# Optimization experiments

Hardware: AMD Instinct MI355X
Metric: run time of the kernel (lower is better)

The kernel has to match this reference:

```python
import jax, jax.numpy as jnp
import numpy as np

NUM_HEADS = 16

def setup_inputs() -> dict:
    key = jax.random.key(0)
    k1, k2, k3 = jax.random.split(key, 3)
    B, S, D = 4, 4096, 2048
    q = jax.random.normal(k1, (B, S, D), dtype=jnp.float32)
    k = jax.random.normal(k2, (B, S, D), dtype=jnp.float32)
    v = jax.random.normal(k3, (B, S, D), dtype=jnp.float32)
    # buffer: decay per head, shape (1, num_heads, 1), default 0.9 per head
    decay = jnp.full((1, NUM_HEADS, 1), 0.9, dtype=jnp.float32)
    return {"q": q, "k": k, "v": v, "decay": decay}

def reference(q, k, v, decay):
    B, S, D = q.shape
    H = NUM_HEADS
    hd = D // H
    qh = q.reshape(B, S, H, hd)
    kh = k.reshape(B, S, H, hd)
    vh = v.reshape(B, S, H, hd)
    kv = kh * vh                       # [B,S,H,hd] per-step state increment
    kv_t = jnp.moveaxis(kv, 1, 0)      # [S,B,H,hd] scan over time
    d = decay                          # [1,H,1], broadcasts over (B,H,hd)

    def step(r, inc):
        r = d * r + inc                # r: [B,H,hd]
        return r, r

    r0 = jnp.zeros((B, H, hd), dtype=q.dtype)
    _, rs = jax.lax.scan(step, r0, kv_t)   # rs: [S,B,H,hd]
    out = qh * jnp.moveaxis(rs, 0, 1)      # [B,S,H,hd]
    return out.reshape(B, S, D)
```

## Files before the change

### kernel.cpp

```cpp
#include <hip/hip_runtime.h>


namespace {

constexpr int kBlk  = 256;
constexpr int kB    = 4;
constexpr int kS    = 4096;
constexpr int kD    = 2048;
constexpr int kRow  = kD / 4;
constexpr int kNG   = kB * kRow;
constexpr int kC    = 64;
constexpr int kL    = kS / kC;

__global__ __launch_bounds__(kBlk) void chunk_state_kernel(
    const float4* __restrict__ k, const float4* __restrict__ v,
    const float* __restrict__ decay, float4* __restrict__ A) {
  const int tid = blockIdx.x * kBlk + threadIdx.x;
  const int g   = tid & (kNG - 1);
  const int c   = tid >> 11;
  const int b   = g >> 9;
  const int j4  = g & (kRow - 1);
  const int h   = j4 >> 5;
  const float d = decay[h];

  int base = (b * kS + c * kL) * kRow + j4;
  float4 r = make_float4(0.f, 0.f, 0.f, 0.f);
#pragma unroll 4
  for (int i = 0; i < kL; ++i) {
    float4 kk = k[base + i * kRow];
    float4 vv = v[base + i * kRow];
    r.x = fmaf(d, r.x, kk.x * vv.x);
    r.y = fmaf(d, r.y, kk.y * vv.y);
    r.z = fmaf(d, r.z, kk.z * vv.z);
    r.w = fmaf(d, r.w, kk.w * vv.w);
  }
  A[c * kNG + g] = r;
}

__global__ __launch_bounds__(kBlk) void retention_out_kernel(
    const float4* __restrict__ q, const float4* __restrict__ k,
    const float4* __restrict__ v, const float* __restrict__ decay,
    const float4* __restrict__ A, float4* __restrict__ out) {
  const int tid = blockIdx.x * kBlk + threadIdx.x;
  const int g   = tid & (kNG - 1);
  const int c   = tid >> 11;
  const int b   = g >> 9;
  const int j4  = g & (kRow - 1);
  const int h   = j4 >> 5;
  const float d = decay[h];

  float dL = d;
#pragma unroll
  for (int t = 0; t < 6; ++t) dL *= dL;

  float4 r = make_float4(0.f, 0.f, 0.f, 0.f);
  for (int cc = 0; cc < c; ++cc) {
    float4 a = A[cc * kNG + g];
    r.x = fmaf(dL, r.x, a.x);
    r.y = fmaf(dL, r.y, a.y);
    r.z = fmaf(dL, r.z, a.z);
    r.w = fmaf(dL, r.w, a.w);
  }

  int base = (b * kS + c * kL) * kRow + j4;
#pragma unroll 4
  for (int i = 0; i < kL; ++i) {
    float4 qq = q[base + i * kRow];
    float4 kk = k[base + i * kRow];
    float4 vv = v[base + i * kRow];
    r.x = fmaf(d, r.x, kk.x * vv.x);
    r.y = fmaf(d, r.y, kk.y * vv.y);
    r.z = fmaf(d, r.z, kk.z * vv.z);
    r.w = fmaf(d, r.w, kk.w * vv.w);
    float4 o;
    o.x = qq.x * r.x;
    o.y = qq.y * r.y;
    o.z = qq.z * r.z;
    o.w = qq.w * r.w;
    out[base + i * kRow] = o;
  }
}

}

extern "C" void kernel_launch(void* const* d_in, const int* in_sizes, int n_in,
                              void* d_out, int out_size, void* d_ws, size_t ws_size,
                              hipStream_t stream) {
  const float4* q     = (const float4*)d_in[0];
  const float4* k     = (const float4*)d_in[1];
  const float4* v     = (const float4*)d_in[2];
  const float*  decay = (const float*)d_in[3];
  float4* out = (float4*)d_out;
  float4* A   = (float4*)d_ws;

  const int nthreads = kNG * kC;
  const int nblocks  = nthreads / kBlk;

  chunk_state_kernel<<<nblocks, kBlk, 0, stream>>>(k, v, decay, A);
  retention_out_kernel<<<nblocks, kBlk, 0, stream>>>(q, k, v, decay, A, out);
}
```

Measured before the change: 442.7 us.

## Shrink scan chunks to 16 steps and truncate decayed cross-chunk prefix

Chunk length drops from 64 to 16 timesteps, so both kernels launch four times as many threads and hide memory latency better. The prefix over earlier chunk states is cut off once the accumulated decay falls below about 1e-10. That bound is computed at run time from the decay value, so each thread reads only a few chunk states instead of up to all of them. The hot loops are manually unrolled with loads grouped ahead of use, and occupancy hints are added to the launch bounds. In exchange, the workspace for chunk states grows fourfold, with a fallback to 64-step chunks if the workspace is too small. Dropping terms below the cutoff gives a tiny approximation error.

```diff
diff --git a/kernel.cpp b/kernel.cpp
--- a/kernel.cpp
+++ b/kernel.cpp
@@ -3,16 +3,15 @@
 
 namespace {
 
-constexpr int kBlk  = 256;
-constexpr int kB    = 4;
-constexpr int kS    = 4096;
-constexpr int kD    = 2048;
-constexpr int kRow  = kD / 4;
-constexpr int kNG   = kB * kRow;
-constexpr int kC    = 64;
-constexpr int kL    = kS / kC;
+constexpr int kBlk = 256;
+constexpr int kB   = 4;
+constexpr int kS   = 4096;
+constexpr int kD   = 2048;
+constexpr int kRow = kD / 4;
+constexpr int kNG  = kB * kRow;
 
-__global__ __launch_bounds__(kBlk) void chunk_state_kernel(
+template <int KL>
+__global__ __launch_bounds__(kBlk, 8) void chunk_state_kernel(
     const float4* __restrict__ k, const float4* __restrict__ v,
     const float* __restrict__ decay, float4* __restrict__ A) {
   const int tid = blockIdx.x * kBlk + threadIdx.x;
@@ -20,24 +19,39 @@
   const int c   = tid >> 11;
   const int b   = g >> 9;
   const int j4  = g & (kRow - 1);
-  const int h   = j4 >> 5;
-  const float d = decay[h];
+  const float d = decay[j4 >> 5];
 
-  int base = (b * kS + c * kL) * kRow + j4;
+  const float4* kp = k + (b * kS + c * KL) * kRow + j4;
+  const float4* vp = v + (b * kS + c * KL) * kRow + j4;
   float4 r = make_float4(0.f, 0.f, 0.f, 0.f);
 #pragma unroll 4
-  for (int i = 0; i < kL; ++i) {
-    float4 kk = k[base + i * kRow];
-    float4 vv = v[base + i * kRow];
-    r.x = fmaf(d, r.x, kk.x * vv.x);
-    r.y = fmaf(d, r.y, kk.y * vv.y);
-    r.z = fmaf(d, r.z, kk.z * vv.z);
-    r.w = fmaf(d, r.w, kk.w * vv.w);
+  for (int ii = 0; ii < KL / 4; ++ii) {
+    float4 k0 = kp[0 * kRow], k1 = kp[1 * kRow], k2 = kp[2 * kRow], k3 = kp[3 * kRow];
+    float4 v0 = vp[0 * kRow], v1 = vp[1 * kRow], v2 = vp[2 * kRow], v3 = vp[3 * kRow];
+    kp += 4 * kRow;
+    vp += 4 * kRow;
+    r.x = fmaf(d, r.x, k0.x * v0.x);
+    r.y = fmaf(d, r.y, k0.y * v0.y);
+    r.z = fmaf(d, r.z, k0.z * v0.z);
+    r.w = fmaf(d, r.w, k0.w * v0.w);
+    r.x = fmaf(d, r.x, k1.x * v1.x);
+    r.y = fmaf(d, r.y, k1.y * v1.y);
+    r.z = fmaf(d, r.z, k1.z * v1.z);
+    r.w = fmaf(d, r.w, k1.w * v1.w);
+    r.x = fmaf(d, r.x, k2.x * v2.x);
+    r.y = fmaf(d, r.y, k2.y * v2.y);
+    r.z = fmaf(d, r.z, k2.z * v2.z);
+    r.w = fmaf(d, r.w, k2.w * v2.w);
+    r.x = fmaf(d, r.x, k3.x * v3.x);
+    r.y = fmaf(d, r.y, k3.y * v3.y);
+    r.z = fmaf(d, r.z, k3.z * v3.z);
+    r.w = fmaf(d, r.w, k3.w * v3.w);
   }
   A[c * kNG + g] = r;
 }
 
-__global__ __launch_bounds__(kBlk) void retention_out_kernel(
+template <int KL>
+__global__ __launch_bounds__(kBlk, 4) void retention_out_kernel(
     const float4* __restrict__ q, const float4* __restrict__ k,
     const float4* __restrict__ v, const float* __restrict__ decay,
     const float4* __restrict__ A, float4* __restrict__ out) {
@@ -46,38 +60,71 @@
   const int c   = tid >> 11;
   const int b   = g >> 9;
   const int j4  = g & (kRow - 1);
-  const int h   = j4 >> 5;
-  const float d = decay[h];
+  const float d = decay[j4 >> 5];
 
   float dL = d;
+  constexpr int kLog = (KL == 16) ? 4 : 6;
 #pragma unroll
-  for (int t = 0; t < 6; ++t) dL *= dL;
+  for (int t = 0; t < kLog; ++t) dL *= dL;
+
+  int n = c;
+  if (c > 0 && dL < 0.999999f) {
+    float l = __logf(fmaxf(dL, 1e-37f));
+    int need = (int)ceilf(-23.0259f / l);
+    n = need < 1 ? 1 : (need < c ? need : c);
+  }
 
   float4 r = make_float4(0.f, 0.f, 0.f, 0.f);
-  for (int cc = 0; cc < c; ++cc) {
-    float4 a = A[cc * kNG + g];
+  const float4* ap = A + (c - n) * kNG + g;
+#pragma unroll 2
+  for (int i = 0; i < n; ++i) {
+    float4 a = ap[0];
+    ap += kNG;
     r.x = fmaf(dL, r.x, a.x);
     r.y = fmaf(dL, r.y, a.y);
     r.z = fmaf(dL, r.z, a.z);
     r.w = fmaf(dL, r.w, a.w);
   }
 
-  int base = (b * kS + c * kL) * kRow + j4;
+  const int base = (b * kS + c * KL) * kRow + j4;
+  const float4* qp = q + base;
+  const float4* kp = k + base;
+  const float4* vp = v + base;
+  float4* op = out + base;
 #pragma unroll 4
-  for (int i = 0; i < kL; ++i) {
-    float4 qq = q[base + i * kRow];
-    float4 kk = k[base + i * kRow];
-    float4 vv = v[base + i * kRow];
-    r.x = fmaf(d, r.x, kk.x * vv.x);
-    r.y = fmaf(d, r.y, kk.y * vv.y);
-    r.z = fmaf(d, r.z, kk.z * vv.z);
-    r.w = fmaf(d, r.w, kk.w * vv.w);
+  for (int ii = 0; ii < KL / 4; ++ii) {
+    float4 q0 = qp[0 * kRow], q1 = qp[1 * kRow], q2 = qp[2 * kRow], q3 = qp[3 * kRow];
+    float4 k0 = kp[0 * kRow], k1 = kp[1 * kRow], k2 = kp[2 * kRow], k3 = kp[3 * kRow];
+    float4 v0 = vp[0 * kRow], v1 = vp[1 * kRow], v2 = vp[2 * kRow], v3 = vp[3 * kRow];
+    qp += 4 * kRow;
+    kp += 4 * kRow;
+    vp += 4 * kRow;
     float4 o;
-    o.x = qq.x * r.x;
-    o.y = qq.y * r.y;
-    o.z = qq.z * r.z;
-    o.w = qq.w * r.w;
-    out[base + i * kRow] = o;
+    r.x = fmaf(d, r.x, k0.x * v0.x);
+    r.y = fmaf(d, r.y, k0.y * v0.y);
+    r.z = fmaf(d, r.z, k0.z * v0.z);
+    r.w = fmaf(d, r.w, k0.w * v0.w);
+    o.x = q0.x * r.x; o.y = q0.y * r.y; o.z = q0.z * r.z; o.w = q0.w * r.w;
+    op[0 * kRow] = o;
+    r.x = fmaf(d, r.x, k1.x * v1.x);
+    r.y = fmaf(d, r.y, k1.y * v1.y);
+    r.z = fmaf(d, r.z, k1.z * v1.z);
+    r.w = fmaf(d, r.w, k1.w * v1.w);
+    o.x = q1.x * r.x; o.y = q1.y * r.y; o.z = q1.z * r.z; o.w = q1.w * r.w;
+    op[1 * kRow] = o;
+    r.x = fmaf(d, r.x, k2.x * v2.x);
+    r.y = fmaf(d, r.y, k2.y * v2.y);
+    r.z = fmaf(d, r.z, k2.z * v2.z);
+    r.w = fmaf(d, r.w, k2.w * v2.w);
+    o.x = q2.x * r.x; o.y = q2.y * r.y; o.z = q2.z * r.z; o.w = q2.w * r.w;
+    op[2 * kRow] = o;
+    r.x = fmaf(d, r.x, k3.x * v3.x);
+    r.y = fmaf(d, r.y, k3.y * v3.y);
+    r.z = fmaf(d, r.z, k3.z * v3.z);
+    r.w = fmaf(d, r.w, k3.w * v3.w);
+    o.x = q3.x * r.x; o.y = q3.y * r.y; o.z = q3.z * r.z; o.w = q3.w * r.w;
+    op[3 * kRow] = o;
+    op += 4 * kRow;
   }
 }
 
@@ -93,9 +140,16 @@
   float4* out = (float4*)d_out;
   float4* A   = (float4*)d_ws;
 
-  const int nthreads = kNG * kC;
-  const int nblocks  = nthreads / kBlk;
-
-  chunk_state_kernel<<<nblocks, kBlk, 0, stream>>>(k, v, decay, A);
-  retention_out_kernel<<<nblocks, kBlk, 0, stream>>>(q, k, v, decay, A, out);
+  const size_t needA = (size_t)(kS / 16) * kNG * sizeof(float4);
+  if (ws_size >= needA) {
+    constexpr int KL = 16;
+    const int nblocks = kNG * (kS / KL) / kBlk;
+    chunk_state_kernel<KL><<<nblocks, kBlk, 0, stream>>>(k, v, decay, A);
+    retention_out_kernel<KL><<<nblocks, kBlk, 0, stream>>>(q, k, v, decay, A, out);
+  } else {
+    constexpr int KL = 64;
+    const int nblocks = kNG * (kS / KL) / kBlk;
+    chunk_state_kernel<KL><<<nblocks, kBlk, 0, stream>>>(k, v, decay, A);
+    retention_out_kernel<KL><<<nblocks, kBlk, 0, stream>>>(q, k, v, decay, A, out);
+  }
 }
```

After: 452.4 us. 2.2% more time.
